# Kernel tuning notes

Hardware: AMD Instinct MI355X
Metric: run time of the kernel (lower is better)

Reference implementation:

```python
import jax, jax.numpy as jnp
import numpy as np

B, N, NS, C, H = 2, 2048, 2048, 512, 8
HD = C // H
SCALE = HD ** -0.5
NEG = -10000.0


def setup_inputs() -> dict:
    key = jax.random.key(0)
    ks = jax.random.split(key, 9)
    q = jax.random.normal(ks[0], (B, N, C), dtype=jnp.float32)
    k = jax.random.normal(ks[1], (B, NS, C), dtype=jnp.float32)
    v = jax.random.normal(ks[2], (B, NS, C), dtype=jnp.float32)
    # 1.0 marks invalid support positions (gets -10000 added)
    supp_valid_mask = (jax.random.uniform(ks[3], (B, NS)) < 0.2).astype(jnp.float32)
    # binary fg/bg support mask used for cycle consistency
    supp_mask = jax.random.randint(ks[4], (B, NS), 0, 2, dtype=jnp.int32)
    w = 0.02
    Wq = jax.random.normal(ks[5], (C, C), dtype=jnp.float32) * w
    Wk = jax.random.normal(ks[6], (C, C), dtype=jnp.float32) * w
    Wv = jax.random.normal(ks[7], (C, C), dtype=jnp.float32) * w
    Wproj = jax.random.normal(ks[8], (C, C), dtype=jnp.float32) * w
    return {"q": q, "k": k, "v": v, "supp_valid_mask": supp_valid_mask,
            "supp_mask": supp_mask, "Wq": Wq, "Wk": Wk, "Wv": Wv, "Wproj": Wproj}


def reference(q, k, v, supp_valid_mask, supp_mask, Wq, Wk, Wv, Wproj):
    b, n, c = q.shape
    ns = k.shape[1]
    # linear projections (torch Linear: x @ W^T), split heads -> [B,H,N,HD]
    qh = (q @ Wq.T).reshape(b, n, H, HD).transpose(0, 2, 1, 3)
    kh = (k @ Wk.T).reshape(b, ns, H, HD).transpose(0, 2, 1, 3)
    vh = (v @ Wv.T).reshape(b, ns, H, HD).transpose(0, 2, 1, 3)
    attn = jnp.einsum('bhnd,bhmd->bhnm', qh, kh) * SCALE  # [B,H,N,NS]

    # cycle-consistency association (vectorized over heads)
    k2q = jnp.argmax(attn, axis=2)                    # [B,H,NS] idx into N
    q2k = jnp.argmax(attn, axis=3)                    # [B,H,N]  idx into NS
    re_map_idx = jnp.take_along_axis(q2k, k2q, axis=2)  # [B,H,NS]
    sm = jnp.broadcast_to(supp_mask[:, None, :], (b, H, ns))
    re_map_mask = jnp.take_along_axis(sm, re_map_idx, axis=2)
    asso = sm == re_map_mask                          # [B,H,NS] bool

    # mark cycle-inconsistent positions invalid (eval: ass_drop is identity)
    valid = jnp.broadcast_to(supp_valid_mask[:, None, :], (b, H, ns))
    valid = jnp.where(asso, valid, 1.0)

    attn = attn + (valid * NEG)[:, :, None, :]
    attn = jax.nn.softmax(attn, axis=-1)
    x = jnp.einsum('bhnm,bhmd->bhnd', attn, vh)       # [B,H,N,HD]
    x = x.transpose(0, 2, 1, 3).reshape(b, n, c)
    return x @ Wproj.T
```

## Files before the change

### kernel.cpp

```cpp
#include <hip/hip_runtime.h>
#include <hip/hip_bf16.h>
#include <stdint.h>

#define H_ 8
#define NS_ 2048
#define C_ 512
#define HD_ 64
#define SCALE_ 0.125f
#define NEG_ -10000.0f
#define LOG2E_ 1.4426950408889634f
#define MFIX_ 4.0f

typedef _Float16 f16x8_t __attribute__((ext_vector_type(8)));
typedef _Float16 f16x4_t __attribute__((ext_vector_type(4)));
typedef float f32x4_t __attribute__((ext_vector_type(4)));

#define MFMAH(a, b, c) __builtin_amdgcn_mfma_f32_16x16x32_f16(a, b, c, 0, 0, 0)

__device__ inline f16x8_t load_h8(const _Float16* p) {
    return *reinterpret_cast<const f16x8_t*>(p);
}

__device__ inline void gload_lds16(const void* g, void* l) {
    __builtin_amdgcn_global_load_lds(
        (const __attribute__((address_space(1))) unsigned int*)g,
        (__attribute__((address_space(3))) unsigned int*)l, 16, 0, 0);
}

__device__ inline unsigned orderF(float v) {
    unsigned u = __float_as_uint(v);
    return (u & 0x80000000u) ? ~u : (u | 0x80000000u);
}
__device__ inline unsigned long long packVR(float v, int idx) {
    return ((unsigned long long)orderF(v) << 32) | (unsigned)(~idx);
}
__device__ inline unsigned long long max64(unsigned long long a, unsigned long long b) {
    return a > b ? a : b;
}
__device__ inline unsigned long long shflx64(unsigned long long x, int m) {
    unsigned lo = (unsigned)x, hi = (unsigned)(x >> 32);
    lo = __shfl_xor(lo, m, 64);
    hi = __shfl_xor(hi, m, 64);
    return ((unsigned long long)hi << 32) | lo;
}

__global__ __launch_bounds__(256) void wsplit4(
        const float* __restrict__ w0, const float* __restrict__ w1,
        const float* __restrict__ w2, const float* __restrict__ w3,
        _Float16* __restrict__ hi, _Float16* __restrict__ lo)
{
    const int i = blockIdx.x * 256 + threadIdx.x;
    const int y = blockIdx.y;
    const float* src = (y == 0) ? w0 : (y == 1) ? w1 : (y == 2) ? w2 : w3;
    const float4 v = reinterpret_cast<const float4*>(src)[i];
    f16x4_t hv, lv;
    hv[0] = (_Float16)v.x; hv[1] = (_Float16)v.y;
    hv[2] = (_Float16)v.z; hv[3] = (_Float16)v.w;
    lv[0] = (_Float16)(v.x - (float)hv[0]);
    lv[1] = (_Float16)(v.y - (float)hv[1]);
    lv[2] = (_Float16)(v.z - (float)hv[2]);
    lv[3] = (_Float16)(v.w - (float)hv[3]);
    const size_t o = ((size_t)y << 16) + i;
    reinterpret_cast<f16x4_t*>(hi)[o] = hv;
    reinterpret_cast<f16x4_t*>(lo)[o] = lv;
}

__global__ __launch_bounds__(256) void proj_gemm(
        const float* __restrict__ qin, const float* __restrict__ kin,
        const float* __restrict__ vin,
        const _Float16* __restrict__ wHall, const _Float16* __restrict__ wLall,
        _Float16* __restrict__ qhi, _Float16* __restrict__ qlo,
        _Float16* __restrict__ khi, _Float16* __restrict__ klo,
        _Float16* __restrict__ vT)
{
    __shared__ __attribute__((aligned(16))) _Float16 Wsh[2][2][4096];
    const int zz = blockIdx.z;
    const float* A32 = (zz == 0) ? qin : (zz == 1) ? kin : vin;
    const _Float16* Wh = wHall + ((size_t)zz << 18);
    const _Float16* Wl = wLall + ((size_t)zz << 18);
    const int t = threadIdx.x, w = t >> 6, lane = t & 63;
    const int m16 = lane & 15, quad = lane >> 4;
    const int bm = blockIdx.x << 7, bn = blockIdx.y << 6;
    const int r0 = bm + (w << 5) + m16, r1 = r0 + 16;
    const int krow = lane >> 3, kblk = (lane & 7) ^ (krow & 7);
    const int e = m16 & 7;
    const int s00 = (quad ^ e) << 3, s01 = ((4 + quad) ^ e) << 3;
    const f32x4_t z = {0.f, 0.f, 0.f, 0.f};
    f32x4_t acc[2][4];
    #pragma unroll
    for (int rs = 0; rs < 2; rs++)
        #pragma unroll
        for (int tl = 0; tl < 4; tl++) acc[rs][tl] = z;

    auto stageW = [&](int buf, int kc) {
        #pragma unroll
        for (int ci = 0; ci < 4; ci++) {
            const int pp = (w << 2) + ci;
            const int s = pp >> 3, pj = pp & 7;
            const _Float16* src = (s ? Wl : Wh)
                + (size_t)(bn + (pj << 3) + krow) * C_ + kc + (kblk << 3);
            gload_lds16(src, &Wsh[buf][s][pj << 9]);
        }
    };
    auto loadA = [&](int kc, f16x8_t* d) {
        #pragma unroll
        for (int rs = 0; rs < 2; rs++) {
            const float* pr = A32 + (size_t)(rs ? r1 : r0) * C_ + kc + (quad << 3);
            #pragma unroll
            for (int seg = 0; seg < 2; seg++) {
                f16x8_t hv, lv;
                #pragma unroll
                for (int i = 0; i < 8; i++) {
                    const float x = pr[seg * 32 + i];
                    const _Float16 hh = (_Float16)x;
                    hv[i] = hh;
                    lv[i] = (_Float16)(x - (float)hh);
                }
                d[rs * 4 + seg] = hv;
                d[rs * 4 + seg + 2] = lv;
            }
        }
    };

    f16x8_t cA[8], nA[8];
    stageW(0, 0);
    loadA(0, cA);
    for (int ch = 0; ch < 8; ch++) {
        __syncthreads();
        if (ch + 1 < 8) {
            stageW((ch + 1) & 1, (ch + 1) << 6);
            loadA((ch + 1) << 6, nA);
        }
        const _Float16* W0 = Wsh[ch & 1][0];
        const _Float16* W1 = Wsh[ch & 1][1];
        #pragma unroll
        for (int tl = 0; tl < 4; tl++) {
            const int j64 = ((tl << 4) + m16) << 6;
            const f16x8_t bh0 = load_h8(&W0[j64 + s00]);
            const f16x8_t bh1 = load_h8(&W0[j64 + s01]);
            const f16x8_t bl0 = load_h8(&W1[j64 + s00]);
            const f16x8_t bl1 = load_h8(&W1[j64 + s01]);
            f32x4_t c0 = acc[0][tl];
            c0 = MFMAH(cA[0], bh0, c0); c0 = MFMAH(cA[1], bh1, c0);
            c0 = MFMAH(cA[2], bh0, c0); c0 = MFMAH(cA[3], bh1, c0);
            c0 = MFMAH(cA[0], bl0, c0); c0 = MFMAH(cA[1], bl1, c0);
            acc[0][tl] = c0;
            f32x4_t c1 = acc[1][tl];
            c1 = MFMAH(cA[4], bh0, c1); c1 = MFMAH(cA[5], bh1, c1);
            c1 = MFMAH(cA[6], bh0, c1); c1 = MFMAH(cA[7], bh1, c1);
            c1 = MFMAH(cA[4], bl0, c1); c1 = MFMAH(cA[5], bl1, c1);
            acc[1][tl] = c1;
        }
        #pragma unroll
        for (int i = 0; i < 8; i++) cA[i] = nA[i];
    }
    const int by = blockIdx.y;
    _Float16* o1 = (zz == 0) ? qhi : khi;
    _Float16* o2 = (zz == 0) ? qlo : klo;
    #pragma unroll
    for (int rs = 0; rs < 2; rs++) {
        #pragma unroll
        for (int tl = 0; tl < 4; tl++) {
            #pragma unroll
            for (int r = 0; r < 4; r++) {
                const int gr = bm + (w << 5) + (rs << 4) + (quad << 2) + r;
                const float val = acc[rs][tl][r];
                const int b = gr >> 11, n = gr & 2047;
                const int d = (tl << 4) + m16;
                const int bh = (b << 3) + by;
                if (zz == 2) {
                    const int kp = ((n & 15) << 1) | ((n >> 4) & 1);
                    vT[(((size_t)((bh << 6) + (n >> 5)) << 6) + d) * 32 + kp] = (_Float16)val;
                } else {
                    const size_t idx = ((((size_t)bh << 11) + n) << 6) + d;
                    const _Float16 hh = (_Float16)val;
                    o1[idx] = hh;
                    o2[idx] = (_Float16)(val - (float)hh);
                }
            }
        }
    }
}

__global__ __launch_bounds__(256) void argmax_mfma(
        const _Float16* __restrict__ qhi, const _Float16* __restrict__ qlo,
        const _Float16* __restrict__ khi, const _Float16* __restrict__ klo,
        unsigned long long* __restrict__ rowP, unsigned long long* __restrict__ colP)
{
    __shared__ __attribute__((aligned(16))) _Float16 Ksh[2][2][4096];
    __shared__ unsigned long long colbest[512];
    const int bx = blockIdx.x;
    const int bh = ((bx & 7) << 1) | (bx >> 9);
    const int mid = (bx >> 3) & 63;
    const int rt = mid & 15;
    const int ks = mid >> 4;
    const int t = threadIdx.x, w = t >> 6, lane = t & 63;
    const int m16 = lane & 15, quad = lane >> 4;
    const int wrow = (rt << 7) + (w << 5);
    const size_t qoff0 = ((((size_t)bh << 11) + wrow + m16) << 6) + (quad << 3);
    const size_t qoff1 = qoff0 + 1024;
    const f16x8_t a00h = load_h8(qhi + qoff0), a01h = load_h8(qhi + qoff0 + 32);
    const f16x8_t a00l = load_h8(qlo + qoff0), a01l = load_h8(qlo + qoff0 + 32);
    const f16x8_t a10h = load_h8(qhi + qoff1), a11h = load_h8(qhi + qoff1 + 32);
    const f16x8_t a10l = load_h8(qlo + qoff1), a11l = load_h8(qlo + qoff1 + 32);
    for (int c = t; c < 512; c += 256) colbest[c] = 0;
    const int krow = lane >> 3, kblk = (lane & 7) ^ (krow & 7);
    const int e = m16 & 7;
    const int s00 = (quad ^ e) << 3, s01 = ((4 + quad) ^ e) << 3;
    const size_t kbase = (((size_t)bh << 11) + (ks << 9)) << 6;
    float bv0[4] = {-3.4e38f, -3.4e38f, -3.4e38f, -3.4e38f};
    float bv1[4] = {-3.4e38f, -3.4e38f, -3.4e38f, -3.4e38f};
    int bc0[4] = {0, 0, 0, 0}, bc1[4] = {0, 0, 0, 0};
    const f32x4_t z = {0.f, 0.f, 0.f, 0.f};

    auto stage = [&](int buf, int cidx) {
        const size_t ce = kbase + ((size_t)cidx << 12);
        #pragma unroll
        for (int ci = 0; ci < 4; ci++) {
            const int pp = (w << 2) + ci;
            const int s = pp >> 3, pj = pp & 7;
            const _Float16* src = (s ? klo : khi) + ce + (((pj << 3) + krow) << 6) + (kblk << 3);
            gload_lds16(src, &Ksh[buf][s][pj << 9]);
        }
    };

    stage(0, 0);
    for (int ch = 0; ch < 8; ch++) {
        __syncthreads();
        if (ch + 1 < 8) stage((ch + 1) & 1, ch + 1);
        const _Float16* K0 = Ksh[ch & 1][0];
        const _Float16* K1 = Ksh[ch & 1][1];
        const int kc0 = (ks << 9) + (ch << 6);
        #pragma unroll
        for (int tl = 0; tl < 4; tl++) {
            const int j64 = ((tl << 4) + m16) << 6;
            const f16x8_t bh0 = load_h8(&K0[j64 + s00]);
            const f16x8_t bh1 = load_h8(&K0[j64 + s01]);
            const f16x8_t bl0 = load_h8(&K1[j64 + s00]);
            const f16x8_t bl1 = load_h8(&K1[j64 + s01]);
            f32x4_t c0 = MFMAH(a00h, bh0, z);
            c0 = MFMAH(a01h, bh1, c0);
            c0 = MFMAH(a00l, bh0, c0); c0 = MFMAH(a01l, bh1, c0);
            c0 = MFMAH(a00h, bl0, c0); c0 = MFMAH(a01h, bl1, c0);
            f32x4_t c1 = MFMAH(a10h, bh0, z);
            c1 = MFMAH(a11h, bh1, c1);
            c1 = MFMAH(a10l, bh0, c1); c1 = MFMAH(a11l, bh1, c1);
            c1 = MFMAH(a10h, bl0, c1); c1 = MFMAH(a11h, bl1, c1);
            const int gc = kc0 + (tl << 4) + m16;
            #pragma unroll
            for (int r = 0; r < 4; r++) {
                if (c0[r] > bv0[r]) { bv0[r] = c0[r]; bc0[r] = gc; }
                if (c1[r] > bv1[r]) { bv1[r] = c1[r]; bc1[r] = gc; }
            }
            float v = c0[0]; int ri = (quad << 2);
            if (c0[1] > v) { v = c0[1]; ri = (quad << 2) + 1; }
            if (c0[2] > v) { v = c0[2]; ri = (quad << 2) + 2; }
            if (c0[3] > v) { v = c0[3]; ri = (quad << 2) + 3; }
            if (c1[0] > v) { v = c1[0]; ri = 16 + (quad << 2); }
            if (c1[1] > v) { v = c1[1]; ri = 16 + (quad << 2) + 1; }
            if (c1[2] > v) { v = c1[2]; ri = 16 + (quad << 2) + 2; }
            if (c1[3] > v) { v = c1[3]; ri = 16 + (quad << 2) + 3; }
            unsigned long long pk = packVR(v, wrow + ri);
            pk = max64(pk, shflx64(pk, 16));
            pk = max64(pk, shflx64(pk, 32));
            if (quad == 0) atomicMax(&colbest[(ch << 6) + (tl << 4) + m16], pk);
        }
    }
    #pragma unroll
    for (int r = 0; r < 4; r++) {
        unsigned long long p0 = packVR(bv0[r], bc0[r]);
        p0 = max64(p0, shflx64(p0, 1)); p0 = max64(p0, shflx64(p0, 2));
        p0 = max64(p0, shflx64(p0, 4)); p0 = max64(p0, shflx64(p0, 8));
        if (m16 == 0)
            atomicMax(rowP + ((size_t)bh << 11) + wrow + (quad << 2) + r, p0);
        unsigned long long p1 = packVR(bv1[r], bc1[r]);
        p1 = max64(p1, shflx64(p1, 1)); p1 = max64(p1, shflx64(p1, 2));
        p1 = max64(p1, shflx64(p1, 4)); p1 = max64(p1, shflx64(p1, 8));
        if (m16 == 0)
            atomicMax(rowP + ((size_t)bh << 11) + wrow + 16 + (quad << 2) + r, p1);
    }
    __syncthreads();
    for (int c = t; c < 512; c += 256)
        atomicMax(colP + ((size_t)bh << 11) + (ks << 9) + c, colbest[c]);
}

__global__ __launch_bounds__(256) void resolve(const unsigned long long* __restrict__ q2kP,
        const unsigned long long* __restrict__ k2qP, const int* __restrict__ supp_mask,
        const float* __restrict__ supp_valid, float* __restrict__ vn)
{
    const int t = blockIdx.x * 256 + threadIdx.x;
    const int bh = t >> 11, j = t & 2047, b = bh >> 3;
    const unsigned k2q = 0xFFFFFFFFu - (unsigned)(k2qP[t] & 0xFFFFFFFFull);
    const unsigned rm  = 0xFFFFFFFFu - (unsigned)(q2kP[(bh << 11) + k2q] & 0xFFFFFFFFull);
    const int asso = supp_mask[(b << 11) + j] == supp_mask[(b << 11) + (int)rm];
    const float valid = asso ? supp_valid[(b << 11) + j] : 1.0f;
    vn[t] = fmaf(valid, NEG_ * LOG2E_, -MFIX_);
}

__global__ __launch_bounds__(256) void attn_pv(
        const _Float16* __restrict__ qh, const _Float16* __restrict__ kh,
        const _Float16* __restrict__ vT, const float* __restrict__ vnG,
        float* __restrict__ xp, float* __restrict__ lp)
{
    __shared__ __attribute__((aligned(16))) _Float16 Ksh[2][2048];
    __shared__ __attribute__((aligned(16))) _Float16 Vsh[2][2048];
    __shared__ float vnL[1024];
    __shared__ __attribute__((aligned(16))) unsigned pbuf[4][320];
    const int bx = blockIdx.x;
    const int bh = ((bx & 7) << 1) | (bx >> 9);
    const int mid = (bx >> 3) & 63;
    const int rt = mid & 31, ks = mid >> 5;
    const int t = threadIdx.x, w = t >> 6, lane = t & 63;
    const int m16 = lane & 15, quad = lane >> 4;
    const int rowbase = (rt << 6) + (w << 4);
    const size_t qoff = ((((size_t)bh << 11) + rowbase + m16) << 6) + (quad << 3);
    const f16x8_t a0 = load_h8(qh + qoff), a1 = load_h8(qh + qoff + 32);
    for (int c = t; c < 1024; c += 256) vnL[c] = vnG[(bh << 11) + (ks << 10) + c];
    const float KS = SCALE_ * LOG2E_;
    const int krow = lane >> 3, kblk = (lane & 7) ^ ((lane >> 3) & 7);
    const int vrow = lane >> 2, vblk = (lane & 3) ^ ((lane >> 3) & 3);
    const int e = m16 & 7;
    const int s00 = (quad ^ e) << 3, s01 = ((4 + quad) ^ e) << 3;
    const int vsw = (m16 >> 1) & 3;
    f16x8_t ones;
    #pragma unroll
    for (int i = 0; i < 8; i++) ones[i] = (_Float16)1.0f;
    const f32x4_t z = {0.f, 0.f, 0.f, 0.f};
    f32x4_t xacc[4];
    #pragma unroll
    for (int nt = 0; nt < 4; nt++) xacc[nt] = z;
    f32x4_t lacc = z;
    const size_t kbel = ((size_t)bh << 11) * HD_;
    unsigned* pw = pbuf[w];

    auto stage = [&](int buf, int ch) {
        const int kcg = (ks << 10) + (ch << 5);
        const size_t ce = kbel + (size_t)kcg * HD_;
        const size_t ve = ((size_t)(bh << 6) + (kcg >> 5)) << 11;
        #pragma unroll
        for (int ci = 0; ci < 2; ci++) {
            const int call = (w << 1) + ci;
            if (call < 4) {
                const _Float16* src = kh + ce + ((call * 8 + krow) << 6) + (kblk << 3);
                gload_lds16(src, &Ksh[buf][call << 9]);
            } else {
                const int j = call - 4;
                const _Float16* src = vT + ve + ((j * 16 + vrow) << 5) + (vblk << 3);
                gload_lds16(src, &Vsh[buf][j << 9]);
            }
        }
    };

    stage(0, 0);
    for (int ch = 0; ch < 32; ch++) {
        __syncthreads();
        if (ch + 1 < 32) stage((ch + 1) & 1, ch + 1);
        const _Float16* K = Ksh[ch & 1];
        const _Float16* V = Vsh[ch & 1];
        const f16x8_t b00 = load_h8(&K[(m16 << 6) + s00]);
        const f16x8_t b01 = load_h8(&K[(m16 << 6) + s01]);
        const f16x8_t b10 = load_h8(&K[((16 + m16) << 6) + s00]);
        const f16x8_t b11 = load_h8(&K[((16 + m16) << 6) + s01]);
        f32x4_t c0 = MFMAH(a0, b00, z); c0 = MFMAH(a1, b01, c0);
        f32x4_t c1 = MFMAH(a0, b10, z); c1 = MFMAH(a1, b11, c1);
        const float vn0 = vnL[(ch << 5) + m16], vn1 = vnL[(ch << 5) + 16 + m16];
        #pragma unroll
        for (int r = 0; r < 4; r++) {
            const float p0 = exp2f(fmaf(c0[r], KS, vn0));
            const float p1 = exp2f(fmaf(c1[r], KS, vn1));
            union { _Float16 h[2]; unsigned u; } pk_;
            pk_.h[0] = (_Float16)p0;
            pk_.h[1] = (_Float16)p1;
            pw[((quad << 2) + r) * 20 + m16] = pk_.u;
        }
        __threadfence_block();
        const f16x8_t pa = *reinterpret_cast<const f16x8_t*>(&pw[m16 * 20 + (quad << 2)]);
        lacc = MFMAH(pa, ones, lacc);
        #pragma unroll
        for (int nt = 0; nt < 4; nt++) {
            const f16x8_t vb = load_h8(&V[((nt * 16 + m16) << 5) + ((quad ^ vsw) << 3)]);
            xacc[nt] = MFMAH(pa, vb, xacc[nt]);
        }
    }
    const int b = bh >> 3, h = bh & 7;
    if (m16 == 0) {
        #pragma unroll
        for (int r = 0; r < 4; r++)
            lp[((size_t)ks << 15) + (bh << 11) + rowbase + (quad << 2) + r] = lacc[r];
    }
    const size_t xbase = ((size_t)ks << 21);
    #pragma unroll
    for (int r = 0; r < 4; r++) {
        const int row = rowbase + (quad << 2) + r;
        #pragma unroll
        for (int nt = 0; nt < 4; nt++)
            xp[xbase + (((size_t)(b << 11) + row) << 9) + (h << 6) + (nt << 4) + m16] = xacc[nt][r];
    }
}

__global__ __launch_bounds__(256) void out_gemm(
        const float* __restrict__ xp, const float* __restrict__ lp,
        const _Float16* __restrict__ Wh, const _Float16* __restrict__ Wl,
        float* __restrict__ outF)
{
    __shared__ __attribute__((aligned(16))) _Float16 Wsh[2][2][4096];
    const int t = threadIdx.x, w = t >> 6, lane = t & 63;
    const int m16 = lane & 15, quad = lane >> 4;
    const int bm = blockIdx.x << 7, bn = blockIdx.y << 6;
    const int r0 = bm + (w << 5) + m16, r1 = r0 + 16;
    const int krow = lane >> 3, kblk = (lane & 7) ^ (krow & 7);
    const int e = m16 & 7;
    const int s00 = (quad ^ e) << 3, s01 = ((4 + quad) ^ e) << 3;
    const f32x4_t z = {0.f, 0.f, 0.f, 0.f};
    f32x4_t acc[2][4];
    #pragma unroll
    for (int rs = 0; rs < 2; rs++)
        #pragma unroll
        for (int tl = 0; tl < 4; tl++) acc[rs][tl] = z;

    auto stageW = [&](int buf, int kc) {
        #pragma unroll
        for (int ci = 0; ci < 4; ci++) {
            const int pp = (w << 2) + ci;
            const int s = pp >> 3, pj = pp & 7;
            const _Float16* src = (s ? Wl : Wh)
                + (size_t)(bn + (pj << 3) + krow) * C_ + kc + (kblk << 3);
            gload_lds16(src, &Wsh[buf][s][pj << 9]);
        }
    };
    auto loadA = [&](int ch, f16x8_t* d) {
        const int kc = ch << 6;
        #pragma unroll
        for (int rs = 0; rs < 2; rs++) {
            const int r = rs ? r1 : r0;
            const int b = r >> 11, n = r & 2047;
            const size_t li = ((size_t)((b << 3) + ch) << 11) + n;
            const float linv = 1.0f / (lp[li] + lp[32768 + li]);
            const size_t base = ((size_t)r << 9) + kc + (quad << 3);
            #pragma unroll
            for (int seg = 0; seg < 2; seg++) {
                f16x8_t hv, lv;
                #pragma unroll
                for (int i = 0; i < 8; i++) {
                    const size_t o = base + seg * 32 + i;
                    const float x = (xp[o] + xp[2097152 + o]) * linv;
                    const _Float16 hh = (_Float16)x;
                    hv[i] = hh;
                    lv[i] = (_Float16)(x - (float)hh);
                }
                d[rs * 4 + seg] = hv;
                d[rs * 4 + seg + 2] = lv;
            }
        }
    };

    f16x8_t cA[8], nA[8];
    stageW(0, 0);
    loadA(0, cA);
    for (int ch = 0; ch < 8; ch++) {
        __syncthreads();
        if (ch + 1 < 8) {
            stageW((ch + 1) & 1, (ch + 1) << 6);
            loadA(ch + 1, nA);
        }
        const _Float16* W0 = Wsh[ch & 1][0];
        const _Float16* W1 = Wsh[ch & 1][1];
        #pragma unroll
        for (int tl = 0; tl < 4; tl++) {
            const int j64 = ((tl << 4) + m16) << 6;
            const f16x8_t bh0 = load_h8(&W0[j64 + s00]);
            const f16x8_t bh1 = load_h8(&W0[j64 + s01]);
            const f16x8_t bl0 = load_h8(&W1[j64 + s00]);
            const f16x8_t bl1 = load_h8(&W1[j64 + s01]);
            f32x4_t c0 = acc[0][tl];
            c0 = MFMAH(cA[0], bh0, c0); c0 = MFMAH(cA[1], bh1, c0);
            c0 = MFMAH(cA[2], bh0, c0); c0 = MFMAH(cA[3], bh1, c0);
            c0 = MFMAH(cA[0], bl0, c0); c0 = MFMAH(cA[1], bl1, c0);
            acc[0][tl] = c0;
            f32x4_t c1 = acc[1][tl];
            c1 = MFMAH(cA[4], bh0, c1); c1 = MFMAH(cA[5], bh1, c1);
            c1 = MFMAH(cA[6], bh0, c1); c1 = MFMAH(cA[7], bh1, c1);
            c1 = MFMAH(cA[4], bl0, c1); c1 = MFMAH(cA[5], bl1, c1);
            acc[1][tl] = c1;
        }
        #pragma unroll
        for (int i = 0; i < 8; i++) cA[i] = nA[i];
    }
    #pragma unroll
    for (int rs = 0; rs < 2; rs++) {
        #pragma unroll
        for (int tl = 0; tl < 4; tl++) {
            #pragma unroll
            for (int r = 0; r < 4; r++) {
                const int gr = bm + (w << 5) + (rs << 4) + (quad << 2) + r;
                const int gj = bn + (tl << 4) + m16;
                outF[(size_t)gr * C_ + gj] = acc[rs][tl][r];
            }
        }
    }
}

extern "C" void kernel_launch(void* const* d_in, const int* in_sizes, int n_in,
                              void* d_out, int out_size, void* d_ws, size_t ws_size,
                              hipStream_t stream) {
    const float* q  = (const float*)d_in[0];
    const float* k  = (const float*)d_in[1];
    const float* v  = (const float*)d_in[2];
    const float* supp_valid = (const float*)d_in[3];
    const int*   supp_mask  = (const int*)d_in[4];
    const float* Wq = (const float*)d_in[5];
    const float* Wk = (const float*)d_in[6];
    const float* Wv = (const float*)d_in[7];
    const float* Wp = (const float*)d_in[8];
    float* out = (float*)d_out;

    char* p = (char*)d_ws;
    _Float16* qhi = (_Float16*)p;      p += 4194304;
    _Float16* qlo = (_Float16*)p;      p += 4194304;
    _Float16* khi = (_Float16*)p;      p += 4194304;
    _Float16* klo = (_Float16*)p;      p += 4194304;
    _Float16* vT  = (_Float16*)p;      p += 4194304;
    float* xp     = (float*)p;         p += 16777216;
    _Float16* wH  = (_Float16*)p;      p += 2097152;
    _Float16* wL  = (_Float16*)p;      p += 2097152;
    unsigned long long* q2kP = (unsigned long long*)p; p += 262144;
    unsigned long long* k2qP = (unsigned long long*)p; p += 262144;
    float* lp = (float*)p;             p += 262144;
    float* validNeg = (float*)p;       p += 131072;

    hipMemsetAsync(q2kP, 0, 524288, stream);

    dim3 bG(256);
    wsplit4<<<dim3(256, 4), bG, 0, stream>>>(Wq, Wk, Wv, Wp, wH, wL);
    proj_gemm<<<dim3(32, 8, 3), bG, 0, stream>>>(q, k, v, wH, wL,
                                                 qhi, qlo, khi, klo, vT);

    argmax_mfma<<<1024, bG, 0, stream>>>(qhi, qlo, khi, klo, q2kP, k2qP);

    resolve<<<128, bG, 0, stream>>>(q2kP, k2qP, supp_mask, supp_valid, validNeg);

    attn_pv<<<1024, bG, 0, stream>>>(qhi, khi, vT, validNeg, xp, lp);

    out_gemm<<<dim3(32, 8), bG, 0, stream>>>(xp, lp,
                                             wH + 3 * 262144, wL + 3 * 262144, out);
}
```

Baseline: 221.9 us.

## Drop LDS staging in argmax/attn kernels, load K/V directly with 32x32 register tiles

Both argmax_mfma and attn_pv stop staging K (and V) through LDS with global_load_lds double buffering and instead load B fragments straight from global memory into registers. Each wave now computes a 32x32 tile per step to reuse the loaded fragments. attn_pv switches from a 2-way to a 4-way split over keys, with out_gemm summing four partials. The workspace is re-laid out so xp aliases qlo/klo, which are dead by then. This is meant to remove LDS traffic and barriers, at the cost of uncoalesced-ish global loads, higher register pressure, and extra partial-sum traffic.

After: 277.5 us. 25.1% more time.

```diff
diff --git a/kernel.cpp b/kernel.cpp
--- a/kernel.cpp
+++ b/kernel.cpp
@@ -182,89 +182,89 @@
     }
 }
 
-__global__ __launch_bounds__(256) void argmax_mfma(
+__global__ __launch_bounds__(256, 4) void argmax_mfma(
         const _Float16* __restrict__ qhi, const _Float16* __restrict__ qlo,
         const _Float16* __restrict__ khi, const _Float16* __restrict__ klo,
         unsigned long long* __restrict__ rowP, unsigned long long* __restrict__ colP)
 {
-    __shared__ __attribute__((aligned(16))) _Float16 Ksh[2][2][4096];
     __shared__ unsigned long long colbest[512];
     const int bx = blockIdx.x;
     const int bh = ((bx & 7) << 1) | (bx >> 9);
     const int mid = (bx >> 3) & 63;
-    const int rt = mid & 15;
-    const int ks = mid >> 4;
+    const int rt = mid & 15, ks = mid >> 4;
     const int t = threadIdx.x, w = t >> 6, lane = t & 63;
     const int m16 = lane & 15, quad = lane >> 4;
     const int wrow = (rt << 7) + (w << 5);
-    const size_t qoff0 = ((((size_t)bh << 11) + wrow + m16) << 6) + (quad << 3);
-    const size_t qoff1 = qoff0 + 1024;
-    const f16x8_t a00h = load_h8(qhi + qoff0), a01h = load_h8(qhi + qoff0 + 32);
-    const f16x8_t a00l = load_h8(qlo + qoff0), a01l = load_h8(qlo + qoff0 + 32);
-    const f16x8_t a10h = load_h8(qhi + qoff1), a11h = load_h8(qhi + qoff1 + 32);
-    const f16x8_t a10l = load_h8(qlo + qoff1), a11l = load_h8(qlo + qoff1 + 32);
+    const size_t qoff = ((((size_t)bh << 11) + wrow + m16) << 6) + (quad << 3);
+    const f16x8_t a00h = load_h8(qhi + qoff),        a01h = load_h8(qhi + qoff + 32);
+    const f16x8_t a00l = load_h8(qlo + qoff),        a01l = load_h8(qlo + qoff + 32);
+    const f16x8_t a10h = load_h8(qhi + qoff + 1024), a11h = load_h8(qhi + qoff + 1056);
+    const f16x8_t a10l = load_h8(qlo + qoff + 1024), a11l = load_h8(qlo + qoff + 1056);
     for (int c = t; c < 512; c += 256) colbest[c] = 0;
-    const int krow = lane >> 3, kblk = (lane & 7) ^ (krow & 7);
-    const int e = m16 & 7;
-    const int s00 = (quad ^ e) << 3, s01 = ((4 + quad) ^ e) << 3;
-    const size_t kbase = (((size_t)bh << 11) + (ks << 9)) << 6;
+    __syncthreads();
+    const size_t kofs = ((((size_t)bh << 11) + (ks << 9) + m16) << 6) + (quad << 3);
+    const _Float16* kph = khi + kofs;
+    const _Float16* kpl = klo + kofs;
     float bv0[4] = {-3.4e38f, -3.4e38f, -3.4e38f, -3.4e38f};
     float bv1[4] = {-3.4e38f, -3.4e38f, -3.4e38f, -3.4e38f};
     int bc0[4] = {0, 0, 0, 0}, bc1[4] = {0, 0, 0, 0};
     const f32x4_t z = {0.f, 0.f, 0.f, 0.f};
 
-    auto stage = [&](int buf, int cidx) {
-        const size_t ce = kbase + ((size_t)cidx << 12);
-        #pragma unroll
-        for (int ci = 0; ci < 4; ci++) {
-            const int pp = (w << 2) + ci;
-            const int s = pp >> 3, pj = pp & 7;
-            const _Float16* src = (s ? klo : khi) + ce + (((pj << 3) + krow) << 6) + (kblk << 3);
-            gload_lds16(src, &Ksh[buf][s][pj << 9]);
-        }
-    };
-
-    stage(0, 0);
-    for (int ch = 0; ch < 8; ch++) {
-        __syncthreads();
-        if (ch + 1 < 8) stage((ch + 1) & 1, ch + 1);
-        const _Float16* K0 = Ksh[ch & 1][0];
-        const _Float16* K1 = Ksh[ch & 1][1];
-        const int kc0 = (ks << 9) + (ch << 6);
-        #pragma unroll
-        for (int tl = 0; tl < 4; tl++) {
-            const int j64 = ((tl << 4) + m16) << 6;
-            const f16x8_t bh0 = load_h8(&K0[j64 + s00]);
-            const f16x8_t bh1 = load_h8(&K0[j64 + s01]);
-            const f16x8_t bl0 = load_h8(&K1[j64 + s00]);
-            const f16x8_t bl1 = load_h8(&K1[j64 + s01]);
-            f32x4_t c0 = MFMAH(a00h, bh0, z);
-            c0 = MFMAH(a01h, bh1, c0);
-            c0 = MFMAH(a00l, bh0, c0); c0 = MFMAH(a01l, bh1, c0);
-            c0 = MFMAH(a00h, bl0, c0); c0 = MFMAH(a01h, bl1, c0);
-            f32x4_t c1 = MFMAH(a10h, bh0, z);
-            c1 = MFMAH(a11h, bh1, c1);
-            c1 = MFMAH(a10l, bh0, c1); c1 = MFMAH(a11l, bh1, c1);
-            c1 = MFMAH(a10h, bl0, c1); c1 = MFMAH(a11h, bl1, c1);
-            const int gc = kc0 + (tl << 4) + m16;
-            #pragma unroll
-            for (int r = 0; r < 4; r++) {
-                if (c0[r] > bv0[r]) { bv0[r] = c0[r]; bc0[r] = gc; }
-                if (c1[r] > bv1[r]) { bv1[r] = c1[r]; bc1[r] = gc; }
-            }
-            float v = c0[0]; int ri = (quad << 2);
-            if (c0[1] > v) { v = c0[1]; ri = (quad << 2) + 1; }
-            if (c0[2] > v) { v = c0[2]; ri = (quad << 2) + 2; }
-            if (c0[3] > v) { v = c0[3]; ri = (quad << 2) + 3; }
-            if (c1[0] > v) { v = c1[0]; ri = 16 + (quad << 2); }
-            if (c1[1] > v) { v = c1[1]; ri = 16 + (quad << 2) + 1; }
-            if (c1[2] > v) { v = c1[2]; ri = 16 + (quad << 2) + 2; }
-            if (c1[3] > v) { v = c1[3]; ri = 16 + (quad << 2) + 3; }
-            unsigned long long pk = packVR(v, wrow + ri);
-            pk = max64(pk, shflx64(pk, 16));
-            pk = max64(pk, shflx64(pk, 32));
-            if (quad == 0) atomicMax(&colbest[(ch << 6) + (tl << 4) + m16], pk);
-        }
+    for (int ch = 0; ch < 16; ch++) {
+        const size_t co = (size_t)ch << 11;
+        const f16x8_t b00h = load_h8(kph + co);        const f16x8_t b01h = load_h8(kph + co + 32);
+        const f16x8_t b10h = load_h8(kph + co + 1024); const f16x8_t b11h = load_h8(kph + co + 1056);
+        const f16x8_t b00l = load_h8(kpl + co);        const f16x8_t b01l = load_h8(kpl + co + 32);
+        const f16x8_t b10l = load_h8(kpl + co + 1024); const f16x8_t b11l = load_h8(kpl + co + 1056);
+        f32x4_t c0 = MFMAH(a00h, b00h, z);
+        c0 = MFMAH(a01h, b01h, c0);
+        c0 = MFMAH(a00l, b00h, c0); c0 = MFMAH(a01l, b01h, c0);
+        c0 = MFMAH(a00h, b00l, c0); c0 = MFMAH(a01h, b01l, c0);
+        f32x4_t c1 = MFMAH(a00h, b10h, z);
+        c1 = MFMAH(a01h, b11h, c1);
+        c1 = MFMAH(a00l, b10h, c1); c1 = MFMAH(a01l, b11h, c1);
+        c1 = MFMAH(a00h, b10l, c1); c1 = MFMAH(a01h, b11l, c1);
+        f32x4_t c2 = MFMAH(a10h, b00h, z);
+        c2 = MFMAH(a11h, b01h, c2);
+        c2 = MFMAH(a10l, b00h, c2); c2 = MFMAH(a11l, b01h, c2);
+        c2 = MFMAH(a10h, b00l, c2); c2 = MFMAH(a11h, b01l, c2);
+        f32x4_t c3 = MFMAH(a10h, b10h, z);
+        c3 = MFMAH(a11h, b11h, c3);
+        c3 = MFMAH(a10l, b10h, c3); c3 = MFMAH(a11l, b11h, c3);
+        c3 = MFMAH(a10h, b10l, c3); c3 = MFMAH(a11h, b11l, c3);
+        const int gc0 = (ks << 9) + (ch << 5) + m16;
+        const int gc1 = gc0 + 16;
+        #pragma unroll
+        for (int r = 0; r < 4; r++) {
+            if (c0[r] > bv0[r]) { bv0[r] = c0[r]; bc0[r] = gc0; }
+            if (c1[r] > bv0[r]) { bv0[r] = c1[r]; bc0[r] = gc1; }
+            if (c2[r] > bv1[r]) { bv1[r] = c2[r]; bc1[r] = gc0; }
+            if (c3[r] > bv1[r]) { bv1[r] = c3[r]; bc1[r] = gc1; }
+        }
+        float v = c0[0]; int ri = (quad << 2);
+        if (c0[1] > v) { v = c0[1]; ri = (quad << 2) + 1; }
+        if (c0[2] > v) { v = c0[2]; ri = (quad << 2) + 2; }
+        if (c0[3] > v) { v = c0[3]; ri = (quad << 2) + 3; }
+        if (c2[0] > v) { v = c2[0]; ri = 16 + (quad << 2); }
+        if (c2[1] > v) { v = c2[1]; ri = 16 + (quad << 2) + 1; }
+        if (c2[2] > v) { v = c2[2]; ri = 16 + (quad << 2) + 2; }
+        if (c2[3] > v) { v = c2[3]; ri = 16 + (quad << 2) + 3; }
+        unsigned long long pk0 = packVR(v, wrow + ri);
+        pk0 = max64(pk0, shflx64(pk0, 16));
+        pk0 = max64(pk0, shflx64(pk0, 32));
+        v = c1[0]; ri = (quad << 2);
+        if (c1[1] > v) { v = c1[1]; ri = (quad << 2) + 1; }
+        if (c1[2] > v) { v = c1[2]; ri = (quad << 2) + 2; }
+        if (c1[3] > v) { v = c1[3]; ri = (quad << 2) + 3; }
+        if (c3[0] > v) { v = c3[0]; ri = 16 + (quad << 2); }
+        if (c3[1] > v) { v = c3[1]; ri = 16 + (quad << 2) + 1; }
+        if (c3[2] > v) { v = c3[2]; ri = 16 + (quad << 2) + 2; }
+        if (c3[3] > v) { v = c3[3]; ri = 16 + (quad << 2) + 3; }
+        unsigned long long pk1 = packVR(v, wrow + ri);
+        pk1 = max64(pk1, shflx64(pk1, 16));
+        pk1 = max64(pk1, shflx64(pk1, 32));
+        if (quad == 0)      atomicMax(&colbest[(ch << 5) + m16], pk0);
+        else if (quad == 1) atomicMax(&colbest[(ch << 5) + 16 + m16], pk1);
     }
     #pragma unroll
     for (int r = 0; r < 4; r++) {
@@ -297,104 +297,86 @@
     vn[t] = fmaf(valid, NEG_ * LOG2E_, -MFIX_);
 }
 
-__global__ __launch_bounds__(256) void attn_pv(
+__global__ __launch_bounds__(256, 4) void attn_pv(
         const _Float16* __restrict__ qh, const _Float16* __restrict__ kh,
         const _Float16* __restrict__ vT, const float* __restrict__ vnG,
         float* __restrict__ xp, float* __restrict__ lp)
 {
-    __shared__ __attribute__((aligned(16))) _Float16 Ksh[2][2048];
-    __shared__ __attribute__((aligned(16))) _Float16 Vsh[2][2048];
-    __shared__ float vnL[1024];
-    __shared__ __attribute__((aligned(16))) unsigned pbuf[4][320];
+    __shared__ __attribute__((aligned(16))) unsigned pbuf[4][2][320];
     const int bx = blockIdx.x;
     const int bh = ((bx & 7) << 1) | (bx >> 9);
     const int mid = (bx >> 3) & 63;
-    const int rt = mid & 31, ks = mid >> 5;
+    const int rt = mid & 15, ks = mid >> 4;
     const int t = threadIdx.x, w = t >> 6, lane = t & 63;
     const int m16 = lane & 15, quad = lane >> 4;
-    const int rowbase = (rt << 6) + (w << 4);
+    const int rowbase = (rt << 7) + (w << 5);
     const size_t qoff = ((((size_t)bh << 11) + rowbase + m16) << 6) + (quad << 3);
-    const f16x8_t a0 = load_h8(qh + qoff), a1 = load_h8(qh + qoff + 32);
-    for (int c = t; c < 1024; c += 256) vnL[c] = vnG[(bh << 11) + (ks << 10) + c];
+    const f16x8_t a0 = load_h8(qh + qoff),        a1 = load_h8(qh + qoff + 32);
+    const f16x8_t a2 = load_h8(qh + qoff + 1024), a3 = load_h8(qh + qoff + 1056);
     const float KS = SCALE_ * LOG2E_;
-    const int krow = lane >> 3, kblk = (lane & 7) ^ ((lane >> 3) & 7);
-    const int vrow = lane >> 2, vblk = (lane & 3) ^ ((lane >> 3) & 3);
-    const int e = m16 & 7;
-    const int s00 = (quad ^ e) << 3, s01 = ((4 + quad) ^ e) << 3;
-    const int vsw = (m16 >> 1) & 3;
     f16x8_t ones;
     #pragma unroll
     for (int i = 0; i < 8; i++) ones[i] = (_Float16)1.0f;
     const f32x4_t z = {0.f, 0.f, 0.f, 0.f};
-    f32x4_t xacc[4];
-    #pragma unroll
-    for (int nt = 0; nt < 4; nt++) xacc[nt] = z;
-    f32x4_t lacc = z;
-    const size_t kbel = ((size_t)bh << 11) * HD_;
-    unsigned* pw = pbuf[w];
-
-    auto stage = [&](int buf, int ch) {
-        const int kcg = (ks << 10) + (ch << 5);
-        const size_t ce = kbel + (size_t)kcg * HD_;
-        const size_t ve = ((size_t)(bh << 6) + (kcg >> 5)) << 11;
-        #pragma unroll
-        for (int ci = 0; ci < 2; ci++) {
-            const int call = (w << 1) + ci;
-            if (call < 4) {
-                const _Float16* src = kh + ce + ((call * 8 + krow) << 6) + (kblk << 3);
-                gload_lds16(src, &Ksh[buf][call << 9]);
-            } else {
-                const int j = call - 4;
-                const _Float16* src = vT + ve + ((j * 16 + vrow) << 5) + (vblk << 3);
-                gload_lds16(src, &Vsh[buf][j << 9]);
-            }
-        }
-    };
-
-    stage(0, 0);
-    for (int ch = 0; ch < 32; ch++) {
-        __syncthreads();
-        if (ch + 1 < 32) stage((ch + 1) & 1, ch + 1);
-        const _Float16* K = Ksh[ch & 1];
-        const _Float16* V = Vsh[ch & 1];
-        const f16x8_t b00 = load_h8(&K[(m16 << 6) + s00]);
-        const f16x8_t b01 = load_h8(&K[(m16 << 6) + s01]);
-        const f16x8_t b10 = load_h8(&K[((16 + m16) << 6) + s00]);
-        const f16x8_t b11 = load_h8(&K[((16 + m16) << 6) + s01]);
+    f32x4_t xa0[4], xa1[4], la0 = z, la1 = z;
+    #pragma unroll
+    for (int nt = 0; nt < 4; nt++) { xa0[nt] = z; xa1[nt] = z; }
+    const _Float16* kp = kh + ((((size_t)bh << 11) + (ks << 9) + m16) << 6) + (quad << 3);
+    const _Float16* vp = vT + (((size_t)((bh << 6) + (ks << 4)) << 6) + m16) * 32 + (quad << 3);
+    const float* vnp = vnG + (bh << 11) + (ks << 9);
+    unsigned* pw0 = pbuf[w][0];
+    unsigned* pw1 = pbuf[w][1];
+
+    for (int ch = 0; ch < 16; ch++) {
+        const size_t co = (size_t)ch << 11;
+        const f16x8_t b00 = load_h8(kp + co);
+        const f16x8_t b01 = load_h8(kp + co + 32);
+        const f16x8_t b10 = load_h8(kp + co + 1024);
+        const f16x8_t b11 = load_h8(kp + co + 1056);
         f32x4_t c0 = MFMAH(a0, b00, z); c0 = MFMAH(a1, b01, c0);
         f32x4_t c1 = MFMAH(a0, b10, z); c1 = MFMAH(a1, b11, c1);
-        const float vn0 = vnL[(ch << 5) + m16], vn1 = vnL[(ch << 5) + 16 + m16];
+        f32x4_t c2 = MFMAH(a2, b00, z); c2 = MFMAH(a3, b01, c2);
+        f32x4_t c3 = MFMAH(a2, b10, z); c3 = MFMAH(a3, b11, c3);
+        const float vn0 = vnp[(ch << 5) + m16], vn1 = vnp[(ch << 5) + 16 + m16];
         #pragma unroll
         for (int r = 0; r < 4; r++) {
-            const float p0 = exp2f(fmaf(c0[r], KS, vn0));
-            const float p1 = exp2f(fmaf(c1[r], KS, vn1));
-            union { _Float16 h[2]; unsigned u; } pk_;
-            pk_.h[0] = (_Float16)p0;
-            pk_.h[1] = (_Float16)p1;
-            pw[((quad << 2) + r) * 20 + m16] = pk_.u;
+            union { _Float16 h[2]; unsigned u; } pk0, pk1;
+            pk0.h[0] = (_Float16)exp2f(fmaf(c0[r], KS, vn0));
+            pk0.h[1] = (_Float16)exp2f(fmaf(c1[r], KS, vn1));
+            pw0[((quad << 2) + r) * 20 + m16] = pk0.u;
+            pk1.h[0] = (_Float16)exp2f(fmaf(c2[r], KS, vn0));
+            pk1.h[1] = (_Float16)exp2f(fmaf(c3[r], KS, vn1));
+            pw1[((quad << 2) + r) * 20 + m16] = pk1.u;
         }
         __threadfence_block();
-        const f16x8_t pa = *reinterpret_cast<const f16x8_t*>(&pw[m16 * 20 + (quad << 2)]);
-        lacc = MFMAH(pa, ones, lacc);
+        const f16x8_t pa0 = *reinterpret_cast<const f16x8_t*>(&pw0[m16 * 20 + (quad << 2)]);
+        const f16x8_t pa1 = *reinterpret_cast<const f16x8_t*>(&pw1[m16 * 20 + (quad << 2)]);
+        la0 = MFMAH(pa0, ones, la0);
+        la1 = MFMAH(pa1, ones, la1);
         #pragma unroll
         for (int nt = 0; nt < 4; nt++) {
-            const f16x8_t vb = load_h8(&V[((nt * 16 + m16) << 5) + ((quad ^ vsw) << 3)]);
-            xacc[nt] = MFMAH(pa, vb, xacc[nt]);
+            const f16x8_t vb = load_h8(vp + co + (nt << 9));
+            xa0[nt] = MFMAH(pa0, vb, xa0[nt]);
+            xa1[nt] = MFMAH(pa1, vb, xa1[nt]);
         }
     }
     const int b = bh >> 3, h = bh & 7;
     if (m16 == 0) {
         #pragma unroll
-        for (int r = 0; r < 4; r++)
-            lp[((size_t)ks << 15) + (bh << 11) + rowbase + (quad << 2) + r] = lacc[r];
+        for (int r = 0; r < 4; r++) {
+            lp[((size_t)ks << 15) + (bh << 11) + rowbase + (quad << 2) + r] = la0[r];
+            lp[((size_t)ks << 15) + (bh << 11) + rowbase + 16 + (quad << 2) + r] = la1[r];
+        }
     }
     const size_t xbase = ((size_t)ks << 21);
     #pragma unroll
     for (int r = 0; r < 4; r++) {
-        const int row = rowbase + (quad << 2) + r;
-        #pragma unroll
-        for (int nt = 0; nt < 4; nt++)
-            xp[xbase + (((size_t)(b << 11) + row) << 9) + (h << 6) + (nt << 4) + m16] = xacc[nt][r];
+        const int row0 = rowbase + (quad << 2) + r;
+        #pragma unroll
+        for (int nt = 0; nt < 4; nt++) {
+            xp[xbase + (((size_t)(b << 11) + row0) << 9) + (h << 6) + (nt << 4) + m16] = xa0[nt][r];
+            xp[xbase + (((size_t)(b << 11) + row0 + 16) << 9) + (h << 6) + (nt << 4) + m16] = xa1[nt][r];
+        }
     }
 }
 
@@ -435,7 +417,7 @@
             const int r = rs ? r1 : r0;
             const int b = r >> 11, n = r & 2047;
             const size_t li = ((size_t)((b << 3) + ch) << 11) + n;
-            const float linv = 1.0f / (lp[li] + lp[32768 + li]);
+            const float linv = 1.0f / (lp[li] + lp[32768 + li] + lp[65536 + li] + lp[98304 + li]);
             const size_t base = ((size_t)r << 9) + kc + (quad << 3);
             #pragma unroll
             for (int seg = 0; seg < 2; seg++) {
@@ -443,7 +425,7 @@
                 #pragma unroll
                 for (int i = 0; i < 8; i++) {
                     const size_t o = base + seg * 32 + i;
-                    const float x = (xp[o] + xp[2097152 + o]) * linv;
+                    const float x = (xp[o] + xp[2097152 + o] + xp[4194304 + o] + xp[6291456 + o]) * linv;
                     const _Float16 hh = (_Float16)x;
                     hv[i] = hh;
                     lv[i] = (_Float16)(x - (float)hh);
@@ -516,16 +498,17 @@
 
     char* p = (char*)d_ws;
     _Float16* qhi = (_Float16*)p;      p += 4194304;
+    _Float16* khi = (_Float16*)p;      p += 4194304;
+    _Float16* vT  = (_Float16*)p;      p += 4194304;
+    float* xp     = (float*)p;
     _Float16* qlo = (_Float16*)p;      p += 4194304;
-    _Float16* khi = (_Float16*)p;      p += 4194304;
     _Float16* klo = (_Float16*)p;      p += 4194304;
-    _Float16* vT  = (_Float16*)p;      p += 4194304;
-    float* xp     = (float*)p;         p += 16777216;
+    p += 25165824;
     _Float16* wH  = (_Float16*)p;      p += 2097152;
     _Float16* wL  = (_Float16*)p;      p += 2097152;
     unsigned long long* q2kP = (unsigned long long*)p; p += 262144;
     unsigned long long* k2qP = (unsigned long long*)p; p += 262144;
-    float* lp = (float*)p;             p += 262144;
+    float* lp = (float*)p;             p += 524288;
     float* validNeg = (float*)p;       p += 131072;
 
     hipMemsetAsync(q2kP, 0, 524288, stream);
```

## Fuse resolve into attn_pv, retile to 128 rows x 4 key splits, drop memset

Applied to the files above, without the earlier changes.

The separate resolve kernel is removed. Each attn_pv block now computes its own 512-entry slice of the cycle-consistency mask in shared memory. attn_pv is retiled so each warp handles 32 query rows, two MFMA row tiles sharing the K/V fragments, and the key dimension is split four ways instead of two. out_gemm therefore reduces four partial x and l buffers. The hipMemsetAsync is replaced by zeroing inside proj_gemm, and xp is aliased over the qlo/klo workspace. Together these remove two launches and halve K/V LDS traffic per query row, at the cost of more partial-sum traffic in out_gemm and higher register pressure.

Result: no change. 224.6 us (+1.2%).

```diff
diff --git a/kernel.cpp b/kernel.cpp
--- a/kernel.cpp
+++ b/kernel.cpp
@@ -71,10 +71,14 @@
         const _Float16* __restrict__ wHall, const _Float16* __restrict__ wLall,
         _Float16* __restrict__ qhi, _Float16* __restrict__ qlo,
         _Float16* __restrict__ khi, _Float16* __restrict__ klo,
-        _Float16* __restrict__ vT)
+        _Float16* __restrict__ vT, unsigned long long* __restrict__ pinit)
 {
     __shared__ __attribute__((aligned(16))) _Float16 Wsh[2][2][4096];
     const int zz = blockIdx.z;
+    if (zz == 0) {
+        const int bid = (blockIdx.x << 3) + blockIdx.y;
+        pinit[(bid << 8) + threadIdx.x] = 0ull;
+    }
     const float* A32 = (zz == 0) ? qin : (zz == 1) ? kin : vin;
     const _Float16* Wh = wHall + ((size_t)zz << 18);
     const _Float16* Wl = wLall + ((size_t)zz << 18);
@@ -192,8 +196,7 @@
     const int bx = blockIdx.x;
     const int bh = ((bx & 7) << 1) | (bx >> 9);
     const int mid = (bx >> 3) & 63;
-    const int rt = mid & 15;
-    const int ks = mid >> 4;
+    const int rt = mid & 15, ks = mid >> 4;
     const int t = threadIdx.x, w = t >> 6, lane = t & 63;
     const int m16 = lane & 15, quad = lane >> 4;
     const int wrow = (rt << 7) + (w << 5);
@@ -284,38 +287,37 @@
         atomicMax(colP + ((size_t)bh << 11) + (ks << 9) + c, colbest[c]);
 }
 
-__global__ __launch_bounds__(256) void resolve(const unsigned long long* __restrict__ q2kP,
-        const unsigned long long* __restrict__ k2qP, const int* __restrict__ supp_mask,
-        const float* __restrict__ supp_valid, float* __restrict__ vn)
-{
-    const int t = blockIdx.x * 256 + threadIdx.x;
-    const int bh = t >> 11, j = t & 2047, b = bh >> 3;
-    const unsigned k2q = 0xFFFFFFFFu - (unsigned)(k2qP[t] & 0xFFFFFFFFull);
-    const unsigned rm  = 0xFFFFFFFFu - (unsigned)(q2kP[(bh << 11) + k2q] & 0xFFFFFFFFull);
-    const int asso = supp_mask[(b << 11) + j] == supp_mask[(b << 11) + (int)rm];
-    const float valid = asso ? supp_valid[(b << 11) + j] : 1.0f;
-    vn[t] = fmaf(valid, NEG_ * LOG2E_, -MFIX_);
-}
-
-__global__ __launch_bounds__(256) void attn_pv(
+__global__ __launch_bounds__(256, 4) void attn_pv(
         const _Float16* __restrict__ qh, const _Float16* __restrict__ kh,
-        const _Float16* __restrict__ vT, const float* __restrict__ vnG,
+        const _Float16* __restrict__ vT,
+        const unsigned long long* __restrict__ q2kP,
+        const unsigned long long* __restrict__ k2qP,
+        const int* __restrict__ supp_mask, const float* __restrict__ supp_valid,
         float* __restrict__ xp, float* __restrict__ lp)
 {
     __shared__ __attribute__((aligned(16))) _Float16 Ksh[2][2048];
     __shared__ __attribute__((aligned(16))) _Float16 Vsh[2][2048];
-    __shared__ float vnL[1024];
-    __shared__ __attribute__((aligned(16))) unsigned pbuf[4][320];
+    __shared__ float vnL[512];
+    __shared__ __attribute__((aligned(16))) unsigned pbuf[4][2][320];
     const int bx = blockIdx.x;
     const int bh = ((bx & 7) << 1) | (bx >> 9);
     const int mid = (bx >> 3) & 63;
-    const int rt = mid & 31, ks = mid >> 5;
+    const int rt = mid & 15, ks = mid >> 4;
     const int t = threadIdx.x, w = t >> 6, lane = t & 63;
     const int m16 = lane & 15, quad = lane >> 4;
-    const int rowbase = (rt << 6) + (w << 4);
+    const int b = bh >> 3, h = bh & 7;
+    for (int c = t; c < 512; c += 256) {
+        const int j = (ks << 9) + c;
+        const unsigned k2q = ~(unsigned)(k2qP[(bh << 11) + j] & 0xFFFFFFFFull);
+        const unsigned rm  = ~(unsigned)(q2kP[(bh << 11) + k2q] & 0xFFFFFFFFull);
+        const int asso = supp_mask[(b << 11) + j] == supp_mask[(b << 11) + (int)rm];
+        const float valid = asso ? supp_valid[(b << 11) + j] : 1.0f;
+        vnL[c] = fmaf(valid, NEG_ * LOG2E_, -MFIX_);
+    }
+    const int rowbase = (rt << 7) + (w << 5);
     const size_t qoff = ((((size_t)bh << 11) + rowbase + m16) << 6) + (quad << 3);
-    const f16x8_t a0 = load_h8(qh + qoff), a1 = load_h8(qh + qoff + 32);
-    for (int c = t; c < 1024; c += 256) vnL[c] = vnG[(bh << 11) + (ks << 10) + c];
+    const f16x8_t a0 = load_h8(qh + qoff),        a1 = load_h8(qh + qoff + 32);
+    const f16x8_t a2 = load_h8(qh + qoff + 1024), a3 = load_h8(qh + qoff + 1056);
     const float KS = SCALE_ * LOG2E_;
     const int krow = lane >> 3, kblk = (lane & 7) ^ ((lane >> 3) & 7);
     const int vrow = lane >> 2, vblk = (lane & 3) ^ ((lane >> 3) & 3);
@@ -326,15 +328,15 @@
     #pragma unroll
     for (int i = 0; i < 8; i++) ones[i] = (_Float16)1.0f;
     const f32x4_t z = {0.f, 0.f, 0.f, 0.f};
-    f32x4_t xacc[4];
-    #pragma unroll
-    for (int nt = 0; nt < 4; nt++) xacc[nt] = z;
-    f32x4_t lacc = z;
+    f32x4_t xa0[4], xa1[4], la0 = z, la1 = z;
+    #pragma unroll
+    for (int nt = 0; nt < 4; nt++) { xa0[nt] = z; xa1[nt] = z; }
     const size_t kbel = ((size_t)bh << 11) * HD_;
-    unsigned* pw = pbuf[w];
+    unsigned* pw0 = pbuf[w][0];
+    unsigned* pw1 = pbuf[w][1];
 
     auto stage = [&](int buf, int ch) {
-        const int kcg = (ks << 10) + (ch << 5);
+        const int kcg = (ks << 9) + (ch << 5);
         const size_t ce = kbel + (size_t)kcg * HD_;
         const size_t ve = ((size_t)(bh << 6) + (kcg >> 5)) << 11;
         #pragma unroll
@@ -352,9 +354,9 @@
     };
 
     stage(0, 0);
-    for (int ch = 0; ch < 32; ch++) {
+    for (int ch = 0; ch < 16; ch++) {
         __syncthreads();
-        if (ch + 1 < 32) stage((ch + 1) & 1, ch + 1);
+        if (ch + 1 < 16) stage((ch + 1) & 1, ch + 1);
         const _Float16* K = Ksh[ch & 1];
         const _Float16* V = Vsh[ch & 1];
         const f16x8_t b00 = load_h8(&K[(m16 << 6) + s00]);
@@ -363,38 +365,47 @@
         const f16x8_t b11 = load_h8(&K[((16 + m16) << 6) + s01]);
         f32x4_t c0 = MFMAH(a0, b00, z); c0 = MFMAH(a1, b01, c0);
         f32x4_t c1 = MFMAH(a0, b10, z); c1 = MFMAH(a1, b11, c1);
+        f32x4_t c2 = MFMAH(a2, b00, z); c2 = MFMAH(a3, b01, c2);
+        f32x4_t c3 = MFMAH(a2, b10, z); c3 = MFMAH(a3, b11, c3);
         const float vn0 = vnL[(ch << 5) + m16], vn1 = vnL[(ch << 5) + 16 + m16];
         #pragma unroll
         for (int r = 0; r < 4; r++) {
-            const float p0 = exp2f(fmaf(c0[r], KS, vn0));
-            const float p1 = exp2f(fmaf(c1[r], KS, vn1));
-            union { _Float16 h[2]; unsigned u; } pk_;
-            pk_.h[0] = (_Float16)p0;
-            pk_.h[1] = (_Float16)p1;
-            pw[((quad << 2) + r) * 20 + m16] = pk_.u;
+            union { _Float16 hh[2]; unsigned u; } pk0, pk1;
+            pk0.hh[0] = (_Float16)exp2f(fmaf(c0[r], KS, vn0));
+            pk0.hh[1] = (_Float16)exp2f(fmaf(c1[r], KS, vn1));
+            pw0[((quad << 2) + r) * 20 + m16] = pk0.u;
+            pk1.hh[0] = (_Float16)exp2f(fmaf(c2[r], KS, vn0));
+            pk1.hh[1] = (_Float16)exp2f(fmaf(c3[r], KS, vn1));
+            pw1[((quad << 2) + r) * 20 + m16] = pk1.u;
         }
         __threadfence_block();
-        const f16x8_t pa = *reinterpret_cast<const f16x8_t*>(&pw[m16 * 20 + (quad << 2)]);
-        lacc = MFMAH(pa, ones, lacc);
+        const f16x8_t pa0 = *reinterpret_cast<const f16x8_t*>(&pw0[m16 * 20 + (quad << 2)]);
+        const f16x8_t pa1 = *reinterpret_cast<const f16x8_t*>(&pw1[m16 * 20 + (quad << 2)]);
+        la0 = MFMAH(pa0, ones, la0);
+        la1 = MFMAH(pa1, ones, la1);
         #pragma unroll
         for (int nt = 0; nt < 4; nt++) {
             const f16x8_t vb = load_h8(&V[((nt * 16 + m16) << 5) + ((quad ^ vsw) << 3)]);
-            xacc[nt] = MFMAH(pa, vb, xacc[nt]);
-        }
-    }
-    const int b = bh >> 3, h = bh & 7;
+            xa0[nt] = MFMAH(pa0, vb, xa0[nt]);
+            xa1[nt] = MFMAH(pa1, vb, xa1[nt]);
+        }
+    }
     if (m16 == 0) {
         #pragma unroll
-        for (int r = 0; r < 4; r++)
-            lp[((size_t)ks << 15) + (bh << 11) + rowbase + (quad << 2) + r] = lacc[r];
+        for (int r = 0; r < 4; r++) {
+            lp[((size_t)ks << 15) + (bh << 11) + rowbase + (quad << 2) + r] = la0[r];
+            lp[((size_t)ks << 15) + (bh << 11) + rowbase + 16 + (quad << 2) + r] = la1[r];
+        }
     }
     const size_t xbase = ((size_t)ks << 21);
     #pragma unroll
     for (int r = 0; r < 4; r++) {
-        const int row = rowbase + (quad << 2) + r;
-        #pragma unroll
-        for (int nt = 0; nt < 4; nt++)
-            xp[xbase + (((size_t)(b << 11) + row) << 9) + (h << 6) + (nt << 4) + m16] = xacc[nt][r];
+        const int row0 = rowbase + (quad << 2) + r;
+        #pragma unroll
+        for (int nt = 0; nt < 4; nt++) {
+            xp[xbase + (((size_t)(b << 11) + row0) << 9) + (h << 6) + (nt << 4) + m16] = xa0[nt][r];
+            xp[xbase + (((size_t)(b << 11) + row0 + 16) << 9) + (h << 6) + (nt << 4) + m16] = xa1[nt][r];
+        }
     }
 }
 
@@ -435,7 +446,7 @@
             const int r = rs ? r1 : r0;
             const int b = r >> 11, n = r & 2047;
             const size_t li = ((size_t)((b << 3) + ch) << 11) + n;
-            const float linv = 1.0f / (lp[li] + lp[32768 + li]);
+            const float linv = 1.0f / (lp[li] + lp[32768 + li] + lp[65536 + li] + lp[98304 + li]);
             const size_t base = ((size_t)r << 9) + kc + (quad << 3);
             #pragma unroll
             for (int seg = 0; seg < 2; seg++) {
@@ -443,7 +454,7 @@
                 #pragma unroll
                 for (int i = 0; i < 8; i++) {
                     const size_t o = base + seg * 32 + i;
-                    const float x = (xp[o] + xp[2097152 + o]) * linv;
+                    const float x = (xp[o] + xp[2097152 + o] + xp[4194304 + o] + xp[6291456 + o]) * linv;
                     const _Float16 hh = (_Float16)x;
                     hv[i] = hh;
                     lv[i] = (_Float16)(x - (float)hh);
@@ -516,30 +527,27 @@
 
     char* p = (char*)d_ws;
     _Float16* qhi = (_Float16*)p;      p += 4194304;
+    _Float16* khi = (_Float16*)p;      p += 4194304;
+    _Float16* vT  = (_Float16*)p;      p += 4194304;
+    float* xp     = (float*)p;
     _Float16* qlo = (_Float16*)p;      p += 4194304;
-    _Float16* khi = (_Float16*)p;      p += 4194304;
     _Float16* klo = (_Float16*)p;      p += 4194304;
-    _Float16* vT  = (_Float16*)p;      p += 4194304;
-    float* xp     = (float*)p;         p += 16777216;
+    p += 25165824;
     _Float16* wH  = (_Float16*)p;      p += 2097152;
     _Float16* wL  = (_Float16*)p;      p += 2097152;
     unsigned long long* q2kP = (unsigned long long*)p; p += 262144;
     unsigned long long* k2qP = (unsigned long long*)p; p += 262144;
-    float* lp = (float*)p;             p += 262144;
-    float* validNeg = (float*)p;       p += 131072;
-
-    hipMemsetAsync(q2kP, 0, 524288, stream);
+    float* lp = (float*)p;             p += 524288;
 
     dim3 bG(256);
     wsplit4<<<dim3(256, 4), bG, 0, stream>>>(Wq, Wk, Wv, Wp, wH, wL);
     proj_gemm<<<dim3(32, 8, 3), bG, 0, stream>>>(q, k, v, wH, wL,
-                                                 qhi, qlo, khi, klo, vT);
+                                                 qhi, qlo, khi, klo, vT, q2kP);
 
     argmax_mfma<<<1024, bG, 0, stream>>>(qhi, qlo, khi, klo, q2kP, k2qP);
 
-    resolve<<<128, bG, 0, stream>>>(q2kP, k2qP, supp_mask, supp_valid, validNeg);
-
-    attn_pv<<<1024, bG, 0, stream>>>(qhi, khi, vT, validNeg, xp, lp);
+    attn_pv<<<1024, bG, 0, stream>>>(qhi, khi, vT, q2kP, k2qP,
+                                     supp_mask, supp_valid, xp, lp);
 
     out_gemm<<<dim3(32, 8), bG, 0, stream>>>(xp, lp,
                                              wH + 3 * 262144, wL + 3 * 262144, out);
```
